# Optimization experiments

Measured on AMD Instinct MI355X. Metric: run time of the kernel, lower is better.

Reference implementation:

```python
import jax, jax.numpy as jnp
import numpy as np

KERNEL_SIZE = 15  # matches init kwarg


def setup_inputs() -> dict:
    key = jax.random.key(0)
    k1, k2 = jax.random.split(key)
    B, T, C, H, W = 1, 8, 3, 96, 96
    K2 = KERNEL_SIZE * KERNEL_SIZE
    data = jax.random.normal(k1, (B, T, C, H, W), dtype=jnp.float32)
    kernels = jax.random.uniform(k2, (B, T, K2, C, H, W), dtype=jnp.float32)
    return {"data": data, "kernels": kernels}


def reference(data, kernels):
    # data:    [B, T, C, H, W]
    # kernels: [B, T, K*K, C, H, W]
    K = KERNEL_SIZE
    p = K // 2
    H, W = data.shape[-2], data.shape[-1]
    # zero-pad spatial dims (matches F.pad with default mode='constant')
    dp = jnp.pad(data, ((0, 0), (0, 0), (0, 0), (p, p), (p, p)))
    # shift-stack: tap order is i (row offset) major, j (col offset) minor,
    # matching the torch double loop.  stack axis=2 -> [B, T, K*K, C, H, W]
    img_stack = jnp.stack(
        [dp[..., i:i + H, j:j + W] for i in range(K) for j in range(K)],
        axis=2,
    )
    # per-pixel dynamic kernel: multiply and reduce over the K*K taps
    pred_burst = jnp.sum(kernels * img_stack, axis=2)  # [B, T, C, H, W]
    return pred_burst
```

## Files before the change

### kernel.cpp

```cpp
#include <hip/hip_runtime.h>


constexpr int K   = 15;
constexpr int P   = 7;
constexpr int H   = 96;
constexpr int W   = 96;
constexpr int C   = 3;
constexpr int T   = 8;
constexpr int HW  = H * W;
constexpr int K2  = K * K;
constexpr int QW  = W / 4;
constexpr int QPP = H * QW;
constexpr int NQ  = T * C * QPP;
constexpr int BLK = 64;
constexpr int NBLK = NQ / BLK;

__global__ __launch_bounds__(BLK) void kpn_kernel(
    const float* __restrict__ data,
    const float* __restrict__ kern,
    float* __restrict__ out)
{
    const int q = blockIdx.x * BLK + threadIdx.x;

    const int w4    = q % QW;
    const int rem   = q / QW;
    const int h     = rem % H;
    const int plane = rem / H;
    const int t     = plane / C;
    const int c     = plane % C;
    const int wbase = w4 * 4;

    const float* __restrict__ dplane = data + plane * HW;
    const float* __restrict__ kbase =
        kern + ((size_t)(t * K2) * C + (size_t)c) * HW + (size_t)h * W + wbase;
    const size_t kstride = (size_t)C * HW;

    int  colc[K + 3];
    bool cval[K + 3];
    #pragma unroll
    for (int m = 0; m < K + 3; ++m) {
        const int col = wbase - P + m;
        cval[m] = (col >= 0) && (col < W);
        colc[m] = (col < 0) ? 0 : ((col >= W) ? (W - 1) : col);
    }

    float4 acc = make_float4(0.f, 0.f, 0.f, 0.f);

    for (int i = 0; i < K; ++i) {
        const int srow = h + i - P;
        const bool rv  = (srow >= 0) && (srow < H);
        const float* __restrict__ drow = dplane + (rv ? srow : 0) * W;

        float dwin[K + 3];
        #pragma unroll
        for (int m = 0; m < K + 3; ++m) {
            const float v = drow[colc[m]];
            dwin[m] = (rv && cval[m]) ? v : 0.f;
        }

        const float* __restrict__ krow = kbase + (size_t)(i * K) * kstride;

        float4 kv[K];
        #pragma unroll
        for (int j = 0; j < K; ++j) {
            kv[j] = *reinterpret_cast<const float4*>(krow + (size_t)j * kstride);
        }
        #pragma unroll
        for (int j = 0; j < K; ++j) {
            acc.x += kv[j].x * dwin[j + 0];
            acc.y += kv[j].y * dwin[j + 1];
            acc.z += kv[j].z * dwin[j + 2];
            acc.w += kv[j].w * dwin[j + 3];
        }
    }

    *reinterpret_cast<float4*>(out + (size_t)plane * HW + (size_t)h * W + wbase) = acc;
}

extern "C" void kernel_launch(void* const* d_in, const int* in_sizes, int n_in,
                              void* d_out, int out_size, void* d_ws, size_t ws_size,
                              hipStream_t stream) {
    const float* data = (const float*)d_in[0];
    const float* kern = (const float*)d_in[1];
    float* out        = (float*)d_out;
    hipLaunchKernelGGL(kpn_kernel, dim3(NBLK), dim3(BLK), 0, stream,
                       data, kern, out);
}
```

Measured before the change: 291.8 us.

## Double-buffer kernel-weight row loads and use nontemporal loads and stores

Restructures the tap-row loop so that the next row of 15 per-pixel kernel float4 values is loaded into a second register buffer while the current row is being accumulated. The streaming kernel weights are read with nontemporal loads, and the output is written with a nontemporal store, to avoid polluting the cache. The two 15-entry float4 buffers raise register pressure, which may lower occupancy.

New measurement: 275.3 us. 5.6% less time.

```diff
diff --git a/kernel.cpp b/kernel.cpp
--- a/kernel.cpp
+++ b/kernel.cpp
@@ -1,80 +1,95 @@
 #include <hip/hip_runtime.h>
 
 
-constexpr int K   = 15;
-constexpr int P   = 7;
-constexpr int H   = 96;
-constexpr int W   = 96;
-constexpr int C   = 3;
-constexpr int T   = 8;
-constexpr int HW  = H * W;
-constexpr int K2  = K * K;
-constexpr int QW  = W / 4;
-constexpr int QPP = H * QW;
-constexpr int NQ  = T * C * QPP;
-constexpr int BLK = 64;
+typedef float vf4 __attribute__((ext_vector_type(4)));
+
+constexpr int K  = 15;
+constexpr int P  = 7;
+constexpr int H  = 96;
+constexpr int W  = 96;
+constexpr int C  = 3;
+constexpr int T  = 8;
+constexpr int HW = H * W;
+constexpr int K2 = K * K;
+constexpr int NP = T * C;
+constexpr int NE = NP * HW;
+constexpr size_t CHW = (size_t)C * HW;
+constexpr int NQ   = NE / 4;
+constexpr int BLK  = 64;
 constexpr int NBLK = NQ / BLK;
 
-__global__ __launch_bounds__(BLK) void kpn_kernel(
+__device__ __forceinline__ vf4 nt4(const float* p) {
+    return __builtin_nontemporal_load(reinterpret_cast<const vf4*>(p));
+}
+
+__global__ __launch_bounds__(BLK) void kpn_fused_nt(
     const float* __restrict__ data,
     const float* __restrict__ kern,
     float* __restrict__ out)
 {
-    const int q = blockIdx.x * BLK + threadIdx.x;
-
-    const int w4    = q % QW;
-    const int rem   = q / QW;
+    const int q     = blockIdx.x * BLK + threadIdx.x;
+    const int w4    = q % (W / 4);
+    const int rem   = q / (W / 4);
     const int h     = rem % H;
     const int plane = rem / H;
     const int t     = plane / C;
     const int c     = plane % C;
-    const int wbase = w4 * 4;
+    const int col   = w4 * 4;
 
-    const float* __restrict__ dplane = data + plane * HW;
     const float* __restrict__ kbase =
-        kern + ((size_t)(t * K2) * C + (size_t)c) * HW + (size_t)h * W + wbase;
-    const size_t kstride = (size_t)C * HW;
+        kern + ((size_t)(t * K2) * C + (size_t)c) * HW + (size_t)h * W + col;
+    const float* __restrict__ dpl = data + plane * HW;
 
     int  colc[K + 3];
     bool cval[K + 3];
     #pragma unroll
     for (int m = 0; m < K + 3; ++m) {
-        const int col = wbase - P + m;
-        cval[m] = (col >= 0) && (col < W);
-        colc[m] = (col < 0) ? 0 : ((col >= W) ? (W - 1) : col);
+        const int cc = col - P + m;
+        cval[m] = (cc >= 0) && (cc < W);
+        colc[m] = (cc < 0) ? 0 : ((cc >= W) ? (W - 1) : cc);
     }
 
-    float4 acc = make_float4(0.f, 0.f, 0.f, 0.f);
+    float acc[4] = {0.f, 0.f, 0.f, 0.f};
 
-    for (int i = 0; i < K; ++i) {
+    auto load_row = [&](vf4 (&buf)[K], int i) {
+        const float* p = kbase + (size_t)(i * K) * CHW;
+        #pragma unroll
+        for (int j = 0; j < K; ++j) buf[j] = nt4(p + (size_t)j * CHW);
+    };
+
+    auto consume_row = [&](vf4 (&buf)[K], int i) {
         const int srow = h + i - P;
         const bool rv  = (srow >= 0) && (srow < H);
-        const float* __restrict__ drow = dplane + (rv ? srow : 0) * W;
-
+        const float* __restrict__ drow = dpl + (rv ? srow : 0) * W;
         float dwin[K + 3];
         #pragma unroll
         for (int m = 0; m < K + 3; ++m) {
             const float v = drow[colc[m]];
             dwin[m] = (rv && cval[m]) ? v : 0.f;
         }
-
-        const float* __restrict__ krow = kbase + (size_t)(i * K) * kstride;
-
-        float4 kv[K];
         #pragma unroll
         for (int j = 0; j < K; ++j) {
-            kv[j] = *reinterpret_cast<const float4*>(krow + (size_t)j * kstride);
+            acc[0] += buf[j][0] * dwin[j + 0];
+            acc[1] += buf[j][1] * dwin[j + 1];
+            acc[2] += buf[j][2] * dwin[j + 2];
+            acc[3] += buf[j][3] * dwin[j + 3];
         }
-        #pragma unroll
-        for (int j = 0; j < K; ++j) {
-            acc.x += kv[j].x * dwin[j + 0];
-            acc.y += kv[j].y * dwin[j + 1];
-            acc.z += kv[j].z * dwin[j + 2];
-            acc.w += kv[j].w * dwin[j + 3];
-        }
+    };
+
+    vf4 A[K], B[K];
+    load_row(A, 0);
+    #pragma unroll 1
+    for (int i = 0; i < K - 1; i += 2) {
+        load_row(B, i + 1);
+        consume_row(A, i);
+        load_row(A, i + 2);
+        consume_row(B, i + 1);
     }
+    consume_row(A, K - 1);
 
-    *reinterpret_cast<float4*>(out + (size_t)plane * HW + (size_t)h * W + wbase) = acc;
+    vf4 o = { acc[0], acc[1], acc[2], acc[3] };
+    float* op = out + (size_t)plane * HW + (size_t)h * W + col;
+    __builtin_nontemporal_store(o, reinterpret_cast<vf4*>(op));
 }
 
 extern "C" void kernel_launch(void* const* d_in, const int* in_sizes, int n_in,
@@ -83,6 +98,6 @@
     const float* data = (const float*)d_in[0];
     const float* kern = (const float*)d_in[1];
     float* out        = (float*)d_out;
-    hipLaunchKernelGGL(kpn_kernel, dim3(NBLK), dim3(BLK), 0, stream,
+    hipLaunchKernelGGL(kpn_fused_nt, dim3(NBLK), dim3(BLK), 0, stream,
                        data, kern, out);
 }
```
